# Kernel optimization log

Measured on AMD Instinct MI355X. Metric: run time of the kernel, lower is better.

The kernel has to match this reference:

```python
import jax, jax.numpy as jnp
import numpy as np

IMAGE_SIZE = 256
NEAR = 0.1
FAR = 100.0
EPS = 1e-3
BACKGROUND = (0.0, 0.0, 0.0)
CHUNK = 64   # faces per scan step (bounds peak memory of the z-buffer pass)
TINY = 1e-12


def _bary(vx, vy, vz, xp, yp):
    """Barycentric weights / perspective-correct depth at pixel centers.
    vx, vy, vz: 3-tuples of vertex coords, broadcastable with xp/yp.
    Mirrors the CUDA kernel: unnormalized cross-product weights, normalize,
    clamp to [0,1], renormalize, zp = 1 / sum(w_k / z_k), near/far clip."""
    x0, x1, x2 = vx; y0, y1, y2 = vy; z0, z1, z2 = vz
    w0 = yp * (x2 - x1) + xp * (y1 - y2) + (x1 * y2 - x2 * y1)
    w1 = yp * (x0 - x2) + xp * (y2 - y0) + (x2 * y0 - x0 * y2)
    w2 = yp * (x1 - x0) + xp * (y0 - y1) + (x0 * y1 - x1 * y0)
    det = w0 + w1 + w2
    safe_det = jnp.where(jnp.abs(det) > TINY, det, 1.0)
    n0, n1, n2 = w0 / safe_det, w1 / safe_det, w2 / safe_det
    inside = (n0 > 0) & (n1 > 0) & (n2 > 0) & (jnp.abs(det) > TINY)
    n0 = jnp.clip(n0, 0.0, 1.0); n1 = jnp.clip(n1, 0.0, 1.0); n2 = jnp.clip(n2, 0.0, 1.0)
    s = n0 + n1 + n2
    s = jnp.where(s > TINY, s, 1.0)
    n0, n1, n2 = n0 / s, n1 / s, n2 / s
    inv_zp = n0 / z0 + n1 / z1 + n2 / z2
    inv_zp = jnp.where(jnp.abs(inv_zp) > TINY, inv_zp, 1.0)
    zp = 1.0 / inv_zp
    valid = inside & (zp > NEAR) & (zp < FAR)
    return (n0, n1, n2), zp, valid


def _pixel_coords():
    IS = IMAGE_SIZE
    return (2.0 * jnp.arange(IS, dtype=jnp.float32) + 1.0 - IS) / IS


def _forward(faces, textures):
    B, F = faces.shape[:2]
    IS = IMAGE_SIZE
    ii = _pixel_coords()

    # ---- pass 1: z-buffer (face-index argmin), chunked scan over faces ----
    # index selection is non-differentiable -> stop_gradient keeps vjp cheap
    fsg = jax.lax.stop_gradient(faces)
    n_chunks = F // CHUNK
    fchunks = jnp.transpose(fsg.reshape(B, n_chunks, CHUNK, 3, 3), (1, 0, 2, 3, 4))
    bases = jnp.arange(n_chunks, dtype=jnp.int32) * CHUNK
    xp4 = ii[None, None, None, :]
    yp4 = ii[None, None, :, None]

    def step(carry, inp):
        depth, fidx = carry
        fc, base = inp                               # fc: [B, CHUNK, 3, 3]
        vx = tuple(fc[:, :, k, 0][:, :, None, None] for k in range(3))
        vy = tuple(fc[:, :, k, 1][:, :, None, None] for k in range(3))
        vz = tuple(fc[:, :, k, 2][:, :, None, None] for k in range(3))
        _, zp, valid = _bary(vx, vy, vz, xp4, yp4)   # [B, CHUNK, IS, IS]
        zp = jnp.where(valid, zp, jnp.inf)
        local = jnp.argmin(zp, axis=1).astype(jnp.int32)
        zbest = jnp.min(zp, axis=1)
        better = zbest < depth
        depth = jnp.where(better, zbest, depth)
        fidx = jnp.where(better, base + local, fidx)
        return (depth, fidx), None

    init = (jnp.full((B, IS, IS), FAR, jnp.float32),
            jnp.full((B, IS, IS), -1, jnp.int32))
    (_, fidx), _ = jax.lax.scan(step, init, (fchunks, bases))

    # ---- pass 2: differentiable recompute for winning faces ----
    mask = fidx >= 0
    safe_idx = jnp.maximum(fidx, 0)
    fsel = jnp.take_along_axis(
        faces.reshape(B, F, 9), safe_idx.reshape(B, -1, 1), axis=1
    ).reshape(B, IS, IS, 3, 3)
    vx = tuple(fsel[..., k, 0] for k in range(3))
    vy = tuple(fsel[..., k, 1] for k in range(3))
    vz = tuple(fsel[..., k, 2] for k in range(3))
    w, zp, _ = _bary(vx, vy, vz, ii[None, None, :], ii[None, :, None])
    depth_map = jnp.where(mask, zp, FAR)

    # ---- texture sampling: 8-corner trilinear in the T^3 face texel cube ----
    T = textures.shape[2]
    tif = [jnp.clip(w[k] * (T - 1) * zp / vz[k], 0.0, T - 1 - EPS) for k in range(3)]
    lo = [jnp.floor(t) for t in tif]
    fr = [t - l for t, l in zip(tif, lo)]
    lo = [l.astype(jnp.int32) for l in lo]

    tex_flat = textures.reshape(B, F * T * T * T, 3)
    base_idx = safe_idx * (T * T * T)
    rgb = jnp.zeros((B, IS, IS, 3), faces.dtype)
    for d0 in (0, 1):
        for d1 in (0, 1):
            for d2 in (0, 1):
                wgt = ((fr[0] if d0 else 1.0 - fr[0]) *
                       (fr[1] if d1 else 1.0 - fr[1]) *
                       (fr[2] if d2 else 1.0 - fr[2]))
                idx = base_idx + (lo[0] + d0) * T * T + (lo[1] + d1) * T + (lo[2] + d2)
                smp = jnp.take_along_axis(tex_flat, idx.reshape(B, -1, 1), axis=1)
                rgb = rgb + wgt[..., None] * smp.reshape(B, IS, IS, 3)

    bg = jnp.asarray(BACKGROUND, faces.dtype)
    mf = mask.astype(faces.dtype)[..., None]
    rgb_map = rgb * mf + (1.0 - mf) * bg
    alpha_map = mask.astype(faces.dtype)
    # pack (rgb, alpha, depth) into a single [B, IS, IS, 5] tensor
    return jnp.concatenate([rgb_map, alpha_map[..., None], depth_map[..., None]], axis=-1)


def setup_inputs() -> dict:
    key = jax.random.key(0)
    B, F, T = 4, 4096, 4
    k1, k2, k3, k4, k5 = jax.random.split(key, 5)
    # small triangles scattered over the screen with depths in (near, far)
    ctr = jax.random.uniform(k1, (B, F, 1, 2), minval=-0.95, maxval=0.95)
    off = jax.random.uniform(k2, (B, F, 3, 2), minval=-0.08, maxval=0.08)
    xy = ctr + off
    zc = jax.random.uniform(k3, (B, F, 1, 1), minval=1.0, maxval=50.0)
    zo = jax.random.uniform(k4, (B, F, 3, 1), minval=-0.2, maxval=0.2)
    faces = jnp.concatenate([xy, zc + zo], axis=-1).astype(jnp.float32)
    textures = jax.random.uniform(k5, (B, F, T, T, T, 3), dtype=jnp.float32)
    return {"faces": faces, "textures": textures}


def reference(faces, textures):
    return _forward(faces, textures)
```

## Files before the change

kernel.cpp:

```cpp
#include <hip/hip_runtime.h>

#define IS 256
#define FCOUNT 4096
#define NEARP 0.1f
#define FARP 100.0f
#define TINYF 1e-12f
#define CAP 192
#define GCAP 128
#define DET_GLOBAL 1e-5f
#define ZEPS 2e-4f

__device__ __forceinline__ float frn(float r) { asm("" : "+v"(r)); return r; }
__device__ __forceinline__ float mulrn(float a, float b) { return frn(a * b); }
__device__ __forceinline__ float addrn(float a, float b) { return frn(a + b); }
__device__ __forceinline__ float subrn(float a, float b) { return frn(a - b); }
__device__ __forceinline__ float divrn(float a, float b) { return frn(a / b); }
__device__ __forceinline__ float fmarn(float a, float b, float c) {
    return frn(__builtin_fmaf(a, b, c));
}

__global__ __launch_bounds__(64) void bin_kernel(
    const float* __restrict__ faces,
    float4* __restrict__ cA, float4* __restrict__ cB, float4* __restrict__ cC,
    int* __restrict__ counts, int* __restrict__ lists,
    int* __restrict__ gcount, int* __restrict__ glist, int B, int F)
{
    const int gid = blockIdx.x * 64 + threadIdx.x;
    if (gid >= B * F) return;
    const int b = gid >> 12, f = gid & (FCOUNT - 1);
    const float* fp = faces + (size_t)gid * 9;
    const float x0 = fp[0], y0 = fp[1], z0 = fp[2];
    const float x1 = fp[3], y1 = fp[4], z1 = fp[5];
    const float x2 = fp[6], y2 = fp[7], z2 = fp[8];

    const float A0 = subrn(x2, x1), B0 = subrn(y1, y2);
    const float C0 = fmarn(x1, y2, -mulrn(x2, y1));
    const float A1 = subrn(x0, x2), B1 = subrn(y2, y0);
    const float C1 = fmarn(x2, y0, -mulrn(x0, y2));
    const float A2 = subrn(x1, x0), B2 = subrn(y0, y1);
    const float C2 = fmarn(x0, y1, -mulrn(x1, y0));
    cA[gid] = make_float4(A0, B0, C0, A1);
    cB[gid] = make_float4(B1, C1, A2, B2);
    cC[gid] = make_float4(C2, z0, z1, z2);

    const float det = (x1 - x0) * (y2 - y0) - (x2 - x0) * (y1 - y0);
    const float ad = fabsf(det);
    if (ad < DET_GLOBAL) {
        const int pos = atomicAdd(&gcount[b], 1);
        if (pos < GCAP) glist[b * GCAP + pos] = f;
        return;
    }
    const float d = 2e-3f + 3e-7f / ad;
    const float lox = fminf(x0, fminf(x1, x2)) - d;
    const float hix = fmaxf(x0, fmaxf(x1, x2)) + d;
    const float loy = fminf(y0, fminf(y1, y2)) - d;
    const float hiy = fmaxf(y0, fmaxf(y1, y2)) + d;
    int tx0 = (int)ceilf ((256.f * lox + 241.f) * (1.f / 16.f));
    int tx1 = (int)floorf((256.f * hix + 255.f) * (1.f / 16.f));
    int ty0 = (int)ceilf ((256.f * loy + 241.f) * (1.f / 16.f));
    int ty1 = (int)floorf((256.f * hiy + 255.f) * (1.f / 16.f));
    tx0 = max(tx0, 0); tx1 = min(tx1, 31);
    ty0 = max(ty0, 0); ty1 = min(ty1, 31);
    for (int ty = ty0; ty <= ty1; ++ty)
        for (int tx = tx0; tx <= tx1; ++tx) {
            const int t = (b * 32 + ty) * 32 + tx;
            const int pos = atomicAdd(&counts[t], 1);
            if (pos < CAP) lists[(size_t)t * CAP + pos] = f;
        }
}

__global__ __launch_bounds__(256) void raster_kernel(
    const float* __restrict__ faces,
    const float* __restrict__ textures,
    const float4* __restrict__ cA, const float4* __restrict__ cB,
    const float4* __restrict__ cC,
    const int* __restrict__ counts, const int* __restrict__ lists,
    const int* __restrict__ gcount, const int* __restrict__ glist,
    float* __restrict__ out, int B, int F)
{
    const int tid  = threadIdx.x;
    const int lane = tid & 63;
    const int w    = tid >> 6;
    const int b    = blockIdx.x >> 8;
    const int tile = blockIdx.x & 255;
    const int qtx  = 2 * (tile & 15) + (w & 1);
    const int qty  = 2 * (tile >> 4) + (w >> 1);
    const int qbin = (b * 32 + qty) * 32 + qtx;
    const int px   = qtx * 8 + (lane & 7);
    const int py   = qty * 8 + (lane >> 3);
    const float xp = (float)(2 * px + 1 - IS) * (1.0f / IS);
    const float yp = (float)(2 * py + 1 - IS) * (1.0f / IS);

    __shared__ float4 s_a[4][64];
    __shared__ float4 s_b[4][64];
    __shared__ float4 s_c[4][64];
    __shared__ int    s_i[4][64];

    float bestz = FARP;
    int   besti = -1;

    const int cnt  = min(counts[qbin], CAP);
    const int gcnt = min(gcount[b], GCAP);
    const int total = cnt + gcnt;
    const int* mylist = lists + (size_t)qbin * CAP;
    const int* gl     = glist + b * GCAP;
    const int fb = b * F;

    for (int cb = 0; cb < total; cb += 64) {
        const int m = min(total - cb, 64);
        if (lane < m) {
            const int k = cb + lane;
            const int f = (k < cnt) ? mylist[k] : gl[k - cnt];
            s_a[w][lane] = cA[fb + f];
            s_b[w][lane] = cB[fb + f];
            s_c[w][lane] = cC[fb + f];
            s_i[w][lane] = f;
        }
        __builtin_amdgcn_wave_barrier();

        for (int j = 0; j < m; ++j) {
            const float4 fa  = s_a[w][j];
            const float4 fb4 = s_b[w][j];
            const float4 fc  = s_c[w][j];
            const float w0 = addrn(fmarn(yp, fa.x, mulrn(xp, fa.y)), fa.z);
            const float w1 = addrn(fmarn(yp, fa.w, mulrn(xp, fb4.x)), fb4.y);
            const float w2 = addrn(fmarn(yp, fb4.z, mulrn(xp, fb4.w)), fc.x);
            const float det = addrn(addrn(w0, w1), w2);
            bool ins;
            if (det > TINYF)       ins = (w0 > 0.f) && (w1 > 0.f) && (w2 > 0.f);
            else if (det < -TINYF) ins = (w0 < 0.f) && (w1 < 0.f) && (w2 < 0.f);
            else                   ins = false;
            const float minz = fminf(fminf(fc.y, fc.z), fc.w);
            if (ins && minz <= bestz + ZEPS) {
                float n0 = divrn(w0, det), n1 = divrn(w1, det), n2 = divrn(w2, det);
                n0 = frn(fminf(fmaxf(n0, 0.f), 1.f));
                n1 = frn(fminf(fmaxf(n1, 0.f), 1.f));
                n2 = frn(fminf(fmaxf(n2, 0.f), 1.f));
                float s = addrn(addrn(n0, n1), n2);
                s = (s > TINYF) ? s : 1.0f;
                n0 = divrn(n0, s); n1 = divrn(n1, s); n2 = divrn(n2, s);
                float iz = addrn(addrn(divrn(n0, fc.y), divrn(n1, fc.z)),
                                 divrn(n2, fc.w));
                iz = (fabsf(iz) > TINYF) ? iz : 1.0f;
                const float zp = divrn(1.0f, iz);
                if (zp > NEARP && zp < FARP) {
                    const int fi = s_i[w][j];
                    if (zp < bestz || (zp == bestz && fi < besti)) {
                        bestz = zp;
                        besti = fi;
                    }
                }
            }
        }
        __builtin_amdgcn_wave_barrier();
    }

    const float* fbase = faces + (size_t)b * F * 9;
    float r = 0.f, g = 0.f, bch = 0.f, alpha = 0.f, depth = FARP;
    if (besti >= 0) {
        const float* fp = fbase + (size_t)besti * 9;
        const float x0 = fp[0], y0 = fp[1], z0 = fp[2];
        const float x1 = fp[3], y1 = fp[4], z1 = fp[5];
        const float x2 = fp[6], y2 = fp[7], z2 = fp[8];
        const float w0 = addrn(fmarn(yp, subrn(x2, x1), mulrn(xp, subrn(y1, y2))),
                               fmarn(x1, y2, -mulrn(x2, y1)));
        const float w1 = addrn(fmarn(yp, subrn(x0, x2), mulrn(xp, subrn(y2, y0))),
                               fmarn(x2, y0, -mulrn(x0, y2)));
        const float w2 = addrn(fmarn(yp, subrn(x1, x0), mulrn(xp, subrn(y0, y1))),
                               fmarn(x0, y1, -mulrn(x1, y0)));
        const float det = addrn(addrn(w0, w1), w2);
        const float sd = (fabsf(det) > TINYF) ? det : 1.0f;
        float n0 = divrn(w0, sd), n1 = divrn(w1, sd), n2 = divrn(w2, sd);
        n0 = frn(fminf(fmaxf(n0, 0.f), 1.f));
        n1 = frn(fminf(fmaxf(n1, 0.f), 1.f));
        n2 = frn(fminf(fmaxf(n2, 0.f), 1.f));
        float s = addrn(addrn(n0, n1), n2);
        s = (s > TINYF) ? s : 1.0f;
        n0 = divrn(n0, s); n1 = divrn(n1, s); n2 = divrn(n2, s);
        float iz = addrn(addrn(divrn(n0, z0), divrn(n1, z1)), divrn(n2, z2));
        iz = (fabsf(iz) > TINYF) ? iz : 1.0f;
        const float zp = divrn(1.0f, iz);
        depth = zp;

        const float t0 = fminf(fmaxf(divrn(mulrn(mulrn(n0, 3.0f), zp), z0), 0.f), 2.999f);
        const float t1 = fminf(fmaxf(divrn(mulrn(mulrn(n1, 3.0f), zp), z1), 0.f), 2.999f);
        const float t2 = fminf(fmaxf(divrn(mulrn(mulrn(n2, 3.0f), zp), z2), 0.f), 2.999f);
        const float l0 = floorf(t0), l1 = floorf(t1), l2 = floorf(t2);
        const float fr0 = subrn(t0, l0), fr1 = subrn(t1, l1), fr2 = subrn(t2, l2);
        const int i0 = (int)l0, i1 = (int)l1, i2 = (int)l2;

        const float* tx = textures + (size_t)(b * F + besti) * 64 * 3;
        for (int d0 = 0; d0 < 2; ++d0)
            for (int d1 = 0; d1 < 2; ++d1)
                for (int d2 = 0; d2 < 2; ++d2) {
                    const float wg = mulrn(mulrn(d0 ? fr0 : subrn(1.0f, fr0),
                                                 d1 ? fr1 : subrn(1.0f, fr1)),
                                           d2 ? fr2 : subrn(1.0f, fr2));
                    const float* tp = tx + ((i0 + d0) * 16 + (i1 + d1) * 4 + (i2 + d2)) * 3;
                    r   = addrn(r,   mulrn(wg, tp[0]));
                    g   = addrn(g,   mulrn(wg, tp[1]));
                    bch = addrn(bch, mulrn(wg, tp[2]));
                }
        alpha = 1.0f;
    }

    float* op = out + (((size_t)b * IS + py) * IS + px) * 5;
    op[0] = r;
    op[1] = g;
    op[2] = bch;
    op[3] = alpha;
    op[4] = depth;
}

extern "C" void kernel_launch(void* const* d_in, const int* in_sizes, int n_in,
                              void* d_out, int out_size, void* d_ws, size_t ws_size,
                              hipStream_t stream) {
    const float* faces    = (const float*)d_in[0];
    const float* textures = (const float*)d_in[1];
    float* out = (float*)d_out;
    const int F = FCOUNT;
    const int B = in_sizes[0] / (F * 9);
    const int nbins = B * 1024;

    int* counts = (int*)d_ws;
    int* gcount = counts + nbins;
    int* glist  = gcount + B;
    int* lists  = glist + B * GCAP;
    float4* cA  = (float4*)(lists + (size_t)nbins * CAP);
    float4* cB  = cA + (size_t)B * F;
    float4* cC  = cB + (size_t)B * F;

    hipMemsetAsync(counts, 0, (size_t)(nbins + B) * sizeof(int), stream);
    bin_kernel<<<dim3((B * F + 63) / 64), dim3(64), 0, stream>>>(
        faces, cA, cB, cC, counts, lists, gcount, glist, B, F);
    raster_kernel<<<dim3(B * 256), dim3(256), 0, stream>>>(
        faces, textures, cA, cB, cC, counts, lists, gcount, glist, out, B, F);
}
```

Baseline: 99.83 us.

## Fuse memset, binning and raster into one cooperative kernel with grid syncs

Replaces the memset plus two kernel launches with a single cooperative kernel. It zeroes the bin counters, bins the faces with a grid-stride loop, then rasterizes, separating the phases with grid-wide barriers. The aim is to remove launch gaps and inter-kernel drain between the small stages. In exchange it adds two grid syncs and needs all 1024 blocks co-resident (launch_bounds 256,4), which can fail or limit occupancy.

```diff
diff --git a/kernel.cpp b/kernel.cpp
--- a/kernel.cpp
+++ b/kernel.cpp
@@ -1,4 +1,7 @@
 #include <hip/hip_runtime.h>
+#include <hip/hip_cooperative_groups.h>
+
+namespace cg = cooperative_groups;
 
 #define IS 256
 #define FCOUNT 4096
@@ -19,66 +22,68 @@
     return frn(__builtin_fmaf(a, b, c));
 }
 
-__global__ __launch_bounds__(64) void bin_kernel(
+__global__ __launch_bounds__(256, 4) void fused_kernel(
     const float* __restrict__ faces,
+    const float* __restrict__ textures,
     float4* __restrict__ cA, float4* __restrict__ cB, float4* __restrict__ cC,
     int* __restrict__ counts, int* __restrict__ lists,
-    int* __restrict__ gcount, int* __restrict__ glist, int B, int F)
-{
-    const int gid = blockIdx.x * 64 + threadIdx.x;
-    if (gid >= B * F) return;
-    const int b = gid >> 12, f = gid & (FCOUNT - 1);
-    const float* fp = faces + (size_t)gid * 9;
-    const float x0 = fp[0], y0 = fp[1], z0 = fp[2];
-    const float x1 = fp[3], y1 = fp[4], z1 = fp[5];
-    const float x2 = fp[6], y2 = fp[7], z2 = fp[8];
-
-    const float A0 = subrn(x2, x1), B0 = subrn(y1, y2);
-    const float C0 = fmarn(x1, y2, -mulrn(x2, y1));
-    const float A1 = subrn(x0, x2), B1 = subrn(y2, y0);
-    const float C1 = fmarn(x2, y0, -mulrn(x0, y2));
-    const float A2 = subrn(x1, x0), B2 = subrn(y0, y1);
-    const float C2 = fmarn(x0, y1, -mulrn(x1, y0));
-    cA[gid] = make_float4(A0, B0, C0, A1);
-    cB[gid] = make_float4(B1, C1, A2, B2);
-    cC[gid] = make_float4(C2, z0, z1, z2);
-
-    const float det = (x1 - x0) * (y2 - y0) - (x2 - x0) * (y1 - y0);
-    const float ad = fabsf(det);
-    if (ad < DET_GLOBAL) {
-        const int pos = atomicAdd(&gcount[b], 1);
-        if (pos < GCAP) glist[b * GCAP + pos] = f;
-        return;
-    }
-    const float d = 2e-3f + 3e-7f / ad;
-    const float lox = fminf(x0, fminf(x1, x2)) - d;
-    const float hix = fmaxf(x0, fmaxf(x1, x2)) + d;
-    const float loy = fminf(y0, fminf(y1, y2)) - d;
-    const float hiy = fmaxf(y0, fmaxf(y1, y2)) + d;
-    int tx0 = (int)ceilf ((256.f * lox + 241.f) * (1.f / 16.f));
-    int tx1 = (int)floorf((256.f * hix + 255.f) * (1.f / 16.f));
-    int ty0 = (int)ceilf ((256.f * loy + 241.f) * (1.f / 16.f));
-    int ty1 = (int)floorf((256.f * hiy + 255.f) * (1.f / 16.f));
-    tx0 = max(tx0, 0); tx1 = min(tx1, 31);
-    ty0 = max(ty0, 0); ty1 = min(ty1, 31);
-    for (int ty = ty0; ty <= ty1; ++ty)
-        for (int tx = tx0; tx <= tx1; ++tx) {
-            const int t = (b * 32 + ty) * 32 + tx;
-            const int pos = atomicAdd(&counts[t], 1);
-            if (pos < CAP) lists[(size_t)t * CAP + pos] = f;
-        }
-}
-
-__global__ __launch_bounds__(256) void raster_kernel(
-    const float* __restrict__ faces,
-    const float* __restrict__ textures,
-    const float4* __restrict__ cA, const float4* __restrict__ cB,
-    const float4* __restrict__ cC,
-    const int* __restrict__ counts, const int* __restrict__ lists,
-    const int* __restrict__ gcount, const int* __restrict__ glist,
+    int* __restrict__ gcount, int* __restrict__ glist,
     float* __restrict__ out, int B, int F)
 {
-    const int tid  = threadIdx.x;
+    const int tid      = threadIdx.x;
+    const int gid      = blockIdx.x * 256 + tid;
+    const int nthreads = gridDim.x * 256;
+    const int nbins    = B * 1024;
+
+    for (int i = gid; i < nbins + B; i += nthreads) counts[i] = 0;
+
+    cg::this_grid().sync();
+
+    for (int fg = gid; fg < B * F; fg += nthreads) {
+        const int b = fg >> 12, f = fg & (FCOUNT - 1);
+        const float* fp = faces + (size_t)fg * 9;
+        const float x0 = fp[0], y0 = fp[1], z0 = fp[2];
+        const float x1 = fp[3], y1 = fp[4], z1 = fp[5];
+        const float x2 = fp[6], y2 = fp[7], z2 = fp[8];
+
+        const float A0 = subrn(x2, x1), B0 = subrn(y1, y2);
+        const float C0 = fmarn(x1, y2, -mulrn(x2, y1));
+        const float A1 = subrn(x0, x2), B1 = subrn(y2, y0);
+        const float C1 = fmarn(x2, y0, -mulrn(x0, y2));
+        const float A2 = subrn(x1, x0), B2 = subrn(y0, y1);
+        const float C2 = fmarn(x0, y1, -mulrn(x1, y0));
+        cA[fg] = make_float4(A0, B0, C0, A1);
+        cB[fg] = make_float4(B1, C1, A2, B2);
+        cC[fg] = make_float4(C2, z0, z1, z2);
+
+        const float det = (x1 - x0) * (y2 - y0) - (x2 - x0) * (y1 - y0);
+        const float ad = fabsf(det);
+        if (ad < DET_GLOBAL) {
+            const int pos = atomicAdd(&gcount[b], 1);
+            if (pos < GCAP) glist[b * GCAP + pos] = f;
+        } else {
+            const float d = 2e-3f + 3e-7f / ad;
+            const float lox = fminf(x0, fminf(x1, x2)) - d;
+            const float hix = fmaxf(x0, fmaxf(x1, x2)) + d;
+            const float loy = fminf(y0, fminf(y1, y2)) - d;
+            const float hiy = fmaxf(y0, fmaxf(y1, y2)) + d;
+            int tx0 = (int)ceilf ((256.f * lox + 241.f) * (1.f / 16.f));
+            int tx1 = (int)floorf((256.f * hix + 255.f) * (1.f / 16.f));
+            int ty0 = (int)ceilf ((256.f * loy + 241.f) * (1.f / 16.f));
+            int ty1 = (int)floorf((256.f * hiy + 255.f) * (1.f / 16.f));
+            tx0 = max(tx0, 0); tx1 = min(tx1, 31);
+            ty0 = max(ty0, 0); ty1 = min(ty1, 31);
+            for (int ty = ty0; ty <= ty1; ++ty)
+                for (int tx = tx0; tx <= tx1; ++tx) {
+                    const int t = (b * 32 + ty) * 32 + tx;
+                    const int pos = atomicAdd(&counts[t], 1);
+                    if (pos < CAP) lists[(size_t)t * CAP + pos] = f;
+                }
+        }
+    }
+
+    cg::this_grid().sync();
+
     const int lane = tid & 63;
     const int w    = tid >> 6;
     const int b    = blockIdx.x >> 8;
@@ -230,9 +235,13 @@
     float4* cB  = cA + (size_t)B * F;
     float4* cC  = cB + (size_t)B * F;
 
-    hipMemsetAsync(counts, 0, (size_t)(nbins + B) * sizeof(int), stream);
-    bin_kernel<<<dim3((B * F + 63) / 64), dim3(64), 0, stream>>>(
-        faces, cA, cB, cC, counts, lists, gcount, glist, B, F);
-    raster_kernel<<<dim3(B * 256), dim3(256), 0, stream>>>(
-        faces, textures, cA, cB, cC, counts, lists, gcount, glist, out, B, F);
+    int Bv = B, Fv = F;
+    void* args[] = {
+        (void*)&faces, (void*)&textures,
+        (void*)&cA, (void*)&cB, (void*)&cC,
+        (void*)&counts, (void*)&lists, (void*)&gcount, (void*)&glist,
+        (void*)&out, (void*)&Bv, (void*)&Fv
+    };
+    hipLaunchCooperativeKernel((const void*)fused_kernel,
+                               dim3(B * 256), dim3(256), args, 0, stream);
 }
```

Result: slower. 255.8 us (+156.2%).

## Fuse binning into raster kernel with per-block shared-memory face culling

Applied to the files above, without the earlier changes.

Removes the separate memset and global binning kernel with its atomics. Each 256-thread block now scans all 4096 faces of its image, culls them against its 32x32 pixel tile, and stores passing faces in shared memory with a 4-bit quadrant mask. Each wave then loops over that shared list and skips faces whose mask bit does not cover its own 8x8 quadrant. This drops two launches and the global list traffic, but every block re-reads all faces (about 1024 blocks times 147KB) and the per-tile cap of 320 may silently drop faces.

```diff
diff --git a/kernel.cpp b/kernel.cpp
--- a/kernel.cpp
+++ b/kernel.cpp
@@ -5,8 +5,7 @@
 #define NEARP 0.1f
 #define FARP 100.0f
 #define TINYF 1e-12f
-#define CAP 192
-#define GCAP 128
+#define CAP_T 320
 #define DET_GLOBAL 1e-5f
 #define ZEPS 2e-4f
 
@@ -19,63 +18,9 @@
     return frn(__builtin_fmaf(a, b, c));
 }
 
-__global__ __launch_bounds__(64) void bin_kernel(
-    const float* __restrict__ faces,
-    float4* __restrict__ cA, float4* __restrict__ cB, float4* __restrict__ cC,
-    int* __restrict__ counts, int* __restrict__ lists,
-    int* __restrict__ gcount, int* __restrict__ glist, int B, int F)
-{
-    const int gid = blockIdx.x * 64 + threadIdx.x;
-    if (gid >= B * F) return;
-    const int b = gid >> 12, f = gid & (FCOUNT - 1);
-    const float* fp = faces + (size_t)gid * 9;
-    const float x0 = fp[0], y0 = fp[1], z0 = fp[2];
-    const float x1 = fp[3], y1 = fp[4], z1 = fp[5];
-    const float x2 = fp[6], y2 = fp[7], z2 = fp[8];
-
-    const float A0 = subrn(x2, x1), B0 = subrn(y1, y2);
-    const float C0 = fmarn(x1, y2, -mulrn(x2, y1));
-    const float A1 = subrn(x0, x2), B1 = subrn(y2, y0);
-    const float C1 = fmarn(x2, y0, -mulrn(x0, y2));
-    const float A2 = subrn(x1, x0), B2 = subrn(y0, y1);
-    const float C2 = fmarn(x0, y1, -mulrn(x1, y0));
-    cA[gid] = make_float4(A0, B0, C0, A1);
-    cB[gid] = make_float4(B1, C1, A2, B2);
-    cC[gid] = make_float4(C2, z0, z1, z2);
-
-    const float det = (x1 - x0) * (y2 - y0) - (x2 - x0) * (y1 - y0);
-    const float ad = fabsf(det);
-    if (ad < DET_GLOBAL) {
-        const int pos = atomicAdd(&gcount[b], 1);
-        if (pos < GCAP) glist[b * GCAP + pos] = f;
-        return;
-    }
-    const float d = 2e-3f + 3e-7f / ad;
-    const float lox = fminf(x0, fminf(x1, x2)) - d;
-    const float hix = fmaxf(x0, fmaxf(x1, x2)) + d;
-    const float loy = fminf(y0, fminf(y1, y2)) - d;
-    const float hiy = fmaxf(y0, fmaxf(y1, y2)) + d;
-    int tx0 = (int)ceilf ((256.f * lox + 241.f) * (1.f / 16.f));
-    int tx1 = (int)floorf((256.f * hix + 255.f) * (1.f / 16.f));
-    int ty0 = (int)ceilf ((256.f * loy + 241.f) * (1.f / 16.f));
-    int ty1 = (int)floorf((256.f * hiy + 255.f) * (1.f / 16.f));
-    tx0 = max(tx0, 0); tx1 = min(tx1, 31);
-    ty0 = max(ty0, 0); ty1 = min(ty1, 31);
-    for (int ty = ty0; ty <= ty1; ++ty)
-        for (int tx = tx0; tx <= tx1; ++tx) {
-            const int t = (b * 32 + ty) * 32 + tx;
-            const int pos = atomicAdd(&counts[t], 1);
-            if (pos < CAP) lists[(size_t)t * CAP + pos] = f;
-        }
-}
-
-__global__ __launch_bounds__(256) void raster_kernel(
+__global__ __launch_bounds__(256, 4) void fused_raster(
     const float* __restrict__ faces,
     const float* __restrict__ textures,
-    const float4* __restrict__ cA, const float4* __restrict__ cB,
-    const float4* __restrict__ cC,
-    const int* __restrict__ counts, const int* __restrict__ lists,
-    const int* __restrict__ gcount, const int* __restrict__ glist,
     float* __restrict__ out, int B, int F)
 {
     const int tid  = threadIdx.x;
@@ -83,82 +28,122 @@
     const int w    = tid >> 6;
     const int b    = blockIdx.x >> 8;
     const int tile = blockIdx.x & 255;
-    const int qtx  = 2 * (tile & 15) + (w & 1);
-    const int qty  = 2 * (tile >> 4) + (w >> 1);
-    const int qbin = (b * 32 + qty) * 32 + qtx;
-    const int px   = qtx * 8 + (lane & 7);
-    const int py   = qty * 8 + (lane >> 3);
+    const int TX   = tile & 15;
+    const int TY   = tile >> 4;
+
+    __shared__ float4 s_a[CAP_T];
+    __shared__ float4 s_b[CAP_T];
+    __shared__ float4 s_c[CAP_T];
+    __shared__ int    s_i[CAP_T];
+    __shared__ int    s_cnt;
+
+    if (tid == 0) s_cnt = 0;
+    __syncthreads();
+
+    const float qxlo0 = (float)(32 * TX +  1 - 256) * (1.0f / 256.0f);
+    const float qxhi0 = (float)(32 * TX + 15 - 256) * (1.0f / 256.0f);
+    const float qxlo1 = (float)(32 * TX + 17 - 256) * (1.0f / 256.0f);
+    const float qxhi1 = (float)(32 * TX + 31 - 256) * (1.0f / 256.0f);
+    const float qylo0 = (float)(32 * TY +  1 - 256) * (1.0f / 256.0f);
+    const float qyhi0 = (float)(32 * TY + 15 - 256) * (1.0f / 256.0f);
+    const float qylo1 = (float)(32 * TY + 17 - 256) * (1.0f / 256.0f);
+    const float qyhi1 = (float)(32 * TY + 31 - 256) * (1.0f / 256.0f);
+
+    const float* fimg = faces + (size_t)b * F * 9;
+    for (int f = tid; f < F; f += 256) {
+        const float* fp = fimg + (size_t)f * 9;
+        const float x0 = fp[0], y0 = fp[1], z0 = fp[2];
+        const float x1 = fp[3], y1 = fp[4], z1 = fp[5];
+        const float x2 = fp[6], y2 = fp[7], z2 = fp[8];
+
+        const float det = (x1 - x0) * (y2 - y0) - (x2 - x0) * (y1 - y0);
+        const float ad = fabsf(det);
+        int mask;
+        if (ad < DET_GLOBAL) {
+            mask = 0xF;
+        } else {
+            const float d = 2e-3f + 3e-7f / ad;
+            const float lox = fminf(x0, fminf(x1, x2)) - d;
+            const float hix = fmaxf(x0, fmaxf(x1, x2)) + d;
+            const float loy = fminf(y0, fminf(y1, y2)) - d;
+            const float hiy = fmaxf(y0, fmaxf(y1, y2)) + d;
+            const bool ox0 = (hix >= qxlo0) && (lox <= qxhi0);
+            const bool ox1 = (hix >= qxlo1) && (lox <= qxhi1);
+            const bool oy0 = (hiy >= qylo0) && (loy <= qyhi0);
+            const bool oy1 = (hiy >= qylo1) && (loy <= qyhi1);
+            mask = ((ox0 && oy0) ? 1 : 0) | ((ox1 && oy0) ? 2 : 0)
+                 | ((ox0 && oy1) ? 4 : 0) | ((ox1 && oy1) ? 8 : 0);
+        }
+        if (mask) {
+            const float A0 = subrn(x2, x1), B0 = subrn(y1, y2);
+            const float C0 = fmarn(x1, y2, -mulrn(x2, y1));
+            const float A1 = subrn(x0, x2), B1 = subrn(y2, y0);
+            const float C1 = fmarn(x2, y0, -mulrn(x0, y2));
+            const float A2 = subrn(x1, x0), B2 = subrn(y0, y1);
+            const float C2 = fmarn(x0, y1, -mulrn(x1, y0));
+            const int pos = atomicAdd(&s_cnt, 1);
+            if (pos < CAP_T) {
+                s_a[pos] = make_float4(A0, B0, C0, A1);
+                s_b[pos] = make_float4(B1, C1, A2, B2);
+                s_c[pos] = make_float4(C2, z0, z1, z2);
+                s_i[pos] = f | (mask << 12);
+            }
+        }
+    }
+    __syncthreads();
+    const int cnt = min(s_cnt, CAP_T);
+
+    const int qtx = 2 * TX + (w & 1);
+    const int qty = 2 * TY + (w >> 1);
+    const int px  = qtx * 8 + (lane & 7);
+    const int py  = qty * 8 + (lane >> 3);
     const float xp = (float)(2 * px + 1 - IS) * (1.0f / IS);
     const float yp = (float)(2 * py + 1 - IS) * (1.0f / IS);
-
-    __shared__ float4 s_a[4][64];
-    __shared__ float4 s_b[4][64];
-    __shared__ float4 s_c[4][64];
-    __shared__ int    s_i[4][64];
+    const int qbit = 1 << (12 + w);
 
     float bestz = FARP;
     int   besti = -1;
 
-    const int cnt  = min(counts[qbin], CAP);
-    const int gcnt = min(gcount[b], GCAP);
-    const int total = cnt + gcnt;
-    const int* mylist = lists + (size_t)qbin * CAP;
-    const int* gl     = glist + b * GCAP;
-    const int fb = b * F;
-
-    for (int cb = 0; cb < total; cb += 64) {
-        const int m = min(total - cb, 64);
-        if (lane < m) {
-            const int k = cb + lane;
-            const int f = (k < cnt) ? mylist[k] : gl[k - cnt];
-            s_a[w][lane] = cA[fb + f];
-            s_b[w][lane] = cB[fb + f];
-            s_c[w][lane] = cC[fb + f];
-            s_i[w][lane] = f;
-        }
-        __builtin_amdgcn_wave_barrier();
-
-        for (int j = 0; j < m; ++j) {
-            const float4 fa  = s_a[w][j];
-            const float4 fb4 = s_b[w][j];
-            const float4 fc  = s_c[w][j];
-            const float w0 = addrn(fmarn(yp, fa.x, mulrn(xp, fa.y)), fa.z);
-            const float w1 = addrn(fmarn(yp, fa.w, mulrn(xp, fb4.x)), fb4.y);
-            const float w2 = addrn(fmarn(yp, fb4.z, mulrn(xp, fb4.w)), fc.x);
-            const float det = addrn(addrn(w0, w1), w2);
-            bool ins;
-            if (det > TINYF)       ins = (w0 > 0.f) && (w1 > 0.f) && (w2 > 0.f);
-            else if (det < -TINYF) ins = (w0 < 0.f) && (w1 < 0.f) && (w2 < 0.f);
-            else                   ins = false;
-            const float minz = fminf(fminf(fc.y, fc.z), fc.w);
-            if (ins && minz <= bestz + ZEPS) {
-                float n0 = divrn(w0, det), n1 = divrn(w1, det), n2 = divrn(w2, det);
-                n0 = frn(fminf(fmaxf(n0, 0.f), 1.f));
-                n1 = frn(fminf(fmaxf(n1, 0.f), 1.f));
-                n2 = frn(fminf(fmaxf(n2, 0.f), 1.f));
-                float s = addrn(addrn(n0, n1), n2);
-                s = (s > TINYF) ? s : 1.0f;
-                n0 = divrn(n0, s); n1 = divrn(n1, s); n2 = divrn(n2, s);
-                float iz = addrn(addrn(divrn(n0, fc.y), divrn(n1, fc.z)),
-                                 divrn(n2, fc.w));
-                iz = (fabsf(iz) > TINYF) ? iz : 1.0f;
-                const float zp = divrn(1.0f, iz);
-                if (zp > NEARP && zp < FARP) {
-                    const int fi = s_i[w][j];
-                    if (zp < bestz || (zp == bestz && fi < besti)) {
-                        bestz = zp;
-                        besti = fi;
-                    }
+    for (int j = 0; j < cnt; ++j) {
+        const int mi = s_i[j];
+        if (!(mi & qbit)) continue;
+        const float4 fa  = s_a[j];
+        const float4 fb4 = s_b[j];
+        const float4 fc  = s_c[j];
+        const float w0 = addrn(fmarn(yp, fa.x, mulrn(xp, fa.y)), fa.z);
+        const float w1 = addrn(fmarn(yp, fa.w, mulrn(xp, fb4.x)), fb4.y);
+        const float w2 = addrn(fmarn(yp, fb4.z, mulrn(xp, fb4.w)), fc.x);
+        const float det = addrn(addrn(w0, w1), w2);
+        bool ins;
+        if (det > TINYF)       ins = (w0 > 0.f) && (w1 > 0.f) && (w2 > 0.f);
+        else if (det < -TINYF) ins = (w0 < 0.f) && (w1 < 0.f) && (w2 < 0.f);
+        else                   ins = false;
+        const float minz = fminf(fminf(fc.y, fc.z), fc.w);
+        if (ins && minz <= bestz + ZEPS) {
+            float n0 = divrn(w0, det), n1 = divrn(w1, det), n2 = divrn(w2, det);
+            n0 = frn(fminf(fmaxf(n0, 0.f), 1.f));
+            n1 = frn(fminf(fmaxf(n1, 0.f), 1.f));
+            n2 = frn(fminf(fmaxf(n2, 0.f), 1.f));
+            float s = addrn(addrn(n0, n1), n2);
+            s = (s > TINYF) ? s : 1.0f;
+            n0 = divrn(n0, s); n1 = divrn(n1, s); n2 = divrn(n2, s);
+            float iz = addrn(addrn(divrn(n0, fc.y), divrn(n1, fc.z)),
+                             divrn(n2, fc.w));
+            iz = (fabsf(iz) > TINYF) ? iz : 1.0f;
+            const float zp = divrn(1.0f, iz);
+            if (zp > NEARP && zp < FARP) {
+                const int fi = mi & 0xFFF;
+                if (zp < bestz || (zp == bestz && fi < besti)) {
+                    bestz = zp;
+                    besti = fi;
                 }
             }
         }
-        __builtin_amdgcn_wave_barrier();
     }
 
-    const float* fbase = faces + (size_t)b * F * 9;
     float r = 0.f, g = 0.f, bch = 0.f, alpha = 0.f, depth = FARP;
     if (besti >= 0) {
-        const float* fp = fbase + (size_t)besti * 9;
+        const float* fp = fimg + (size_t)besti * 9;
         const float x0 = fp[0], y0 = fp[1], z0 = fp[2];
         const float x1 = fp[3], y1 = fp[4], z1 = fp[5];
         const float x2 = fp[6], y2 = fp[7], z2 = fp[8];
@@ -220,19 +205,7 @@
     float* out = (float*)d_out;
     const int F = FCOUNT;
     const int B = in_sizes[0] / (F * 9);
-    const int nbins = B * 1024;
-
-    int* counts = (int*)d_ws;
-    int* gcount = counts + nbins;
-    int* glist  = gcount + B;
-    int* lists  = glist + B * GCAP;
-    float4* cA  = (float4*)(lists + (size_t)nbins * CAP);
-    float4* cB  = cA + (size_t)B * F;
-    float4* cC  = cB + (size_t)B * F;
-
-    hipMemsetAsync(counts, 0, (size_t)(nbins + B) * sizeof(int), stream);
-    bin_kernel<<<dim3((B * F + 63) / 64), dim3(64), 0, stream>>>(
-        faces, cA, cB, cC, counts, lists, gcount, glist, B, F);
-    raster_kernel<<<dim3(B * 256), dim3(256), 0, stream>>>(
-        faces, textures, cA, cB, cC, counts, lists, gcount, glist, out, B, F);
+
+    fused_raster<<<dim3(B * 256), dim3(256), 0, stream>>>(
+        faces, textures, out, B, F);
 }
```

Result: faster. 96.64 us (median of 2 runs) (-3.2%).

## Stage face loads via LDS in binning, prefetch per-face coefficients in raster

Applied to the files above, without the earlier changes.

The bin kernel now loads each 64-face block's vertex data into shared memory with coalesced float4 loads instead of strided 9-float per-thread reads. The raster kernel switches to one 64-thread block per 8x8 bin and drops the LDS staging and wave barriers. Each face's coefficients are read through uniform global loads with a one-face-ahead software prefetch. The winning face's barycentrics and depths are kept in registers, so the second barycentric recompute from the raw faces is removed. The risks are that the per-face global loads sit on the critical loop with only one face of lookahead, and that each thread now holds more registers.

```diff
diff --git a/kernel.cpp b/kernel.cpp
--- a/kernel.cpp
+++ b/kernel.cpp
@@ -19,16 +19,29 @@
     return frn(__builtin_fmaf(a, b, c));
 }
 
+
 __global__ __launch_bounds__(64) void bin_kernel(
     const float* __restrict__ faces,
     float4* __restrict__ cA, float4* __restrict__ cB, float4* __restrict__ cC,
     int* __restrict__ counts, int* __restrict__ lists,
     int* __restrict__ gcount, int* __restrict__ glist, int B, int F)
 {
-    const int gid = blockIdx.x * 64 + threadIdx.x;
+    const int lane = threadIdx.x;
+    const int base = blockIdx.x * 64;
+    const int gid  = base + lane;
     if (gid >= B * F) return;
     const int b = gid >> 12, f = gid & (FCOUNT - 1);
-    const float* fp = faces + (size_t)gid * 9;
+
+    __shared__ float4 stage4[144];
+    float* stage = (float*)stage4;
+    const float* src = faces + (size_t)base * 9;
+    const float4* s4 = (const float4*)src;
+    stage4[lane]      = s4[lane];
+    stage4[64 + lane] = s4[64 + lane];
+    stage[512 + lane] = src[512 + lane];
+    __builtin_amdgcn_wave_barrier();
+
+    const float* fp = stage + lane * 9;
     const float x0 = fp[0], y0 = fp[1], z0 = fp[2];
     const float x1 = fp[3], y1 = fp[4], z1 = fp[5];
     const float x2 = fp[6], y2 = fp[7], z2 = fp[8];
@@ -69,8 +82,7 @@
         }
 }
 
-__global__ __launch_bounds__(256) void raster_kernel(
-    const float* __restrict__ faces,
+__global__ __launch_bounds__(64) void raster_kernel(
     const float* __restrict__ textures,
     const float4* __restrict__ cA, const float4* __restrict__ cB,
     const float4* __restrict__ cC,
@@ -78,125 +90,96 @@
     const int* __restrict__ gcount, const int* __restrict__ glist,
     float* __restrict__ out, int B, int F)
 {
-    const int tid  = threadIdx.x;
-    const int lane = tid & 63;
-    const int w    = tid >> 6;
-    const int b    = blockIdx.x >> 8;
-    const int tile = blockIdx.x & 255;
-    const int qtx  = 2 * (tile & 15) + (w & 1);
-    const int qty  = 2 * (tile >> 4) + (w >> 1);
-    const int qbin = (b * 32 + qty) * 32 + qtx;
-    const int px   = qtx * 8 + (lane & 7);
-    const int py   = qty * 8 + (lane >> 3);
+    const int lane = threadIdx.x;
+    const int blk  = blockIdx.x;
+    const int b    = blk >> 10;
+    const int tx   = blk & 31;
+    const int ty   = (blk >> 5) & 31;
+    const int bin  = (b * 32 + ty) * 32 + tx;
+    const int px   = tx * 8 + (lane & 7);
+    const int py   = ty * 8 + (lane >> 3);
     const float xp = (float)(2 * px + 1 - IS) * (1.0f / IS);
     const float yp = (float)(2 * py + 1 - IS) * (1.0f / IS);
 
-    __shared__ float4 s_a[4][64];
-    __shared__ float4 s_b[4][64];
-    __shared__ float4 s_c[4][64];
-    __shared__ int    s_i[4][64];
+    const int cnt   = min(counts[bin], CAP);
+    const int gcnt  = min(gcount[b], GCAP);
+    const int total = cnt + gcnt;
+    const int* mylist = lists + (size_t)bin * CAP;
+    const int* gl     = glist + b * GCAP;
+    const int fb = b * F;
 
     float bestz = FARP;
     int   besti = -1;
-
-    const int cnt  = min(counts[qbin], CAP);
-    const int gcnt = min(gcount[b], GCAP);
-    const int total = cnt + gcnt;
-    const int* mylist = lists + (size_t)qbin * CAP;
-    const int* gl     = glist + b * GCAP;
-    const int fb = b * F;
-
-    for (int cb = 0; cb < total; cb += 64) {
-        const int m = min(total - cb, 64);
-        if (lane < m) {
-            const int k = cb + lane;
-            const int f = (k < cnt) ? mylist[k] : gl[k - cnt];
-            s_a[w][lane] = cA[fb + f];
-            s_b[w][lane] = cB[fb + f];
-            s_c[w][lane] = cC[fb + f];
-            s_i[w][lane] = f;
+    float bn0 = 0.f, bn1 = 0.f, bn2 = 0.f;
+    float bz0 = 1.f, bz1 = 1.f, bz2 = 1.f;
+
+    int    pf = 0;
+    float4 pa, pb, pc;
+    if (total > 0) {
+        pf = (0 < cnt) ? mylist[0] : gl[0];
+        pa = cA[fb + pf]; pb = cB[fb + pf]; pc = cC[fb + pf];
+    }
+    for (int j = 0; j < total; ++j) {
+        const float4 fa  = pa;
+        const float4 fb4 = pb;
+        const float4 fc  = pc;
+        const int    fi  = pf;
+        const int jn = j + 1;
+        if (jn < total) {
+            pf = (jn < cnt) ? mylist[jn] : gl[jn - cnt];
+            pa = cA[fb + pf]; pb = cB[fb + pf]; pc = cC[fb + pf];
         }
-        __builtin_amdgcn_wave_barrier();
-
-        for (int j = 0; j < m; ++j) {
-            const float4 fa  = s_a[w][j];
-            const float4 fb4 = s_b[w][j];
-            const float4 fc  = s_c[w][j];
-            const float w0 = addrn(fmarn(yp, fa.x, mulrn(xp, fa.y)), fa.z);
-            const float w1 = addrn(fmarn(yp, fa.w, mulrn(xp, fb4.x)), fb4.y);
-            const float w2 = addrn(fmarn(yp, fb4.z, mulrn(xp, fb4.w)), fc.x);
-            const float det = addrn(addrn(w0, w1), w2);
-            bool ins;
-            if (det > TINYF)       ins = (w0 > 0.f) && (w1 > 0.f) && (w2 > 0.f);
-            else if (det < -TINYF) ins = (w0 < 0.f) && (w1 < 0.f) && (w2 < 0.f);
-            else                   ins = false;
-            const float minz = fminf(fminf(fc.y, fc.z), fc.w);
-            if (ins && minz <= bestz + ZEPS) {
-                float n0 = divrn(w0, det), n1 = divrn(w1, det), n2 = divrn(w2, det);
-                n0 = frn(fminf(fmaxf(n0, 0.f), 1.f));
-                n1 = frn(fminf(fmaxf(n1, 0.f), 1.f));
-                n2 = frn(fminf(fmaxf(n2, 0.f), 1.f));
-                float s = addrn(addrn(n0, n1), n2);
-                s = (s > TINYF) ? s : 1.0f;
-                n0 = divrn(n0, s); n1 = divrn(n1, s); n2 = divrn(n2, s);
-                float iz = addrn(addrn(divrn(n0, fc.y), divrn(n1, fc.z)),
-                                 divrn(n2, fc.w));
-                iz = (fabsf(iz) > TINYF) ? iz : 1.0f;
-                const float zp = divrn(1.0f, iz);
-                if (zp > NEARP && zp < FARP) {
-                    const int fi = s_i[w][j];
-                    if (zp < bestz || (zp == bestz && fi < besti)) {
-                        bestz = zp;
-                        besti = fi;
-                    }
+        const float w0 = addrn(fmarn(yp, fa.x, mulrn(xp, fa.y)), fa.z);
+        const float w1 = addrn(fmarn(yp, fa.w, mulrn(xp, fb4.x)), fb4.y);
+        const float w2 = addrn(fmarn(yp, fb4.z, mulrn(xp, fb4.w)), fc.x);
+        const float det = addrn(addrn(w0, w1), w2);
+        bool ins;
+        if (det > TINYF)       ins = (w0 > 0.f) && (w1 > 0.f) && (w2 > 0.f);
+        else if (det < -TINYF) ins = (w0 < 0.f) && (w1 < 0.f) && (w2 < 0.f);
+        else                   ins = false;
+        const float minz = fminf(fminf(fc.y, fc.z), fc.w);
+        if (ins && minz <= bestz + ZEPS) {
+            float n0 = divrn(w0, det), n1 = divrn(w1, det), n2 = divrn(w2, det);
+            n0 = frn(fminf(fmaxf(n0, 0.f), 1.f));
+            n1 = frn(fminf(fmaxf(n1, 0.f), 1.f));
+            n2 = frn(fminf(fmaxf(n2, 0.f), 1.f));
+            float s = addrn(addrn(n0, n1), n2);
+            s = (s > TINYF) ? s : 1.0f;
+            n0 = divrn(n0, s); n1 = divrn(n1, s); n2 = divrn(n2, s);
+            float iz = addrn(addrn(divrn(n0, fc.y), divrn(n1, fc.z)),
+                             divrn(n2, fc.w));
+            iz = (fabsf(iz) > TINYF) ? iz : 1.0f;
+            const float zp = divrn(1.0f, iz);
+            if (zp > NEARP && zp < FARP) {
+                if (zp < bestz || (zp == bestz && fi < besti)) {
+                    bestz = zp;
+                    besti = fi;
+                    bn0 = n0; bn1 = n1; bn2 = n2;
+                    bz0 = fc.y; bz1 = fc.z; bz2 = fc.w;
                 }
             }
         }
-        __builtin_amdgcn_wave_barrier();
-    }
-
-    const float* fbase = faces + (size_t)b * F * 9;
+    }
+
     float r = 0.f, g = 0.f, bch = 0.f, alpha = 0.f, depth = FARP;
     if (besti >= 0) {
-        const float* fp = fbase + (size_t)besti * 9;
-        const float x0 = fp[0], y0 = fp[1], z0 = fp[2];
-        const float x1 = fp[3], y1 = fp[4], z1 = fp[5];
-        const float x2 = fp[6], y2 = fp[7], z2 = fp[8];
-        const float w0 = addrn(fmarn(yp, subrn(x2, x1), mulrn(xp, subrn(y1, y2))),
-                               fmarn(x1, y2, -mulrn(x2, y1)));
-        const float w1 = addrn(fmarn(yp, subrn(x0, x2), mulrn(xp, subrn(y2, y0))),
-                               fmarn(x2, y0, -mulrn(x0, y2)));
-        const float w2 = addrn(fmarn(yp, subrn(x1, x0), mulrn(xp, subrn(y0, y1))),
-                               fmarn(x0, y1, -mulrn(x1, y0)));
-        const float det = addrn(addrn(w0, w1), w2);
-        const float sd = (fabsf(det) > TINYF) ? det : 1.0f;
-        float n0 = divrn(w0, sd), n1 = divrn(w1, sd), n2 = divrn(w2, sd);
-        n0 = frn(fminf(fmaxf(n0, 0.f), 1.f));
-        n1 = frn(fminf(fmaxf(n1, 0.f), 1.f));
-        n2 = frn(fminf(fmaxf(n2, 0.f), 1.f));
-        float s = addrn(addrn(n0, n1), n2);
-        s = (s > TINYF) ? s : 1.0f;
-        n0 = divrn(n0, s); n1 = divrn(n1, s); n2 = divrn(n2, s);
-        float iz = addrn(addrn(divrn(n0, z0), divrn(n1, z1)), divrn(n2, z2));
-        iz = (fabsf(iz) > TINYF) ? iz : 1.0f;
-        const float zp = divrn(1.0f, iz);
+        const float zp = bestz;
         depth = zp;
-
-        const float t0 = fminf(fmaxf(divrn(mulrn(mulrn(n0, 3.0f), zp), z0), 0.f), 2.999f);
-        const float t1 = fminf(fmaxf(divrn(mulrn(mulrn(n1, 3.0f), zp), z1), 0.f), 2.999f);
-        const float t2 = fminf(fmaxf(divrn(mulrn(mulrn(n2, 3.0f), zp), z2), 0.f), 2.999f);
+        const float t0 = fminf(fmaxf(divrn(mulrn(mulrn(bn0, 3.0f), zp), bz0), 0.f), 2.999f);
+        const float t1 = fminf(fmaxf(divrn(mulrn(mulrn(bn1, 3.0f), zp), bz1), 0.f), 2.999f);
+        const float t2 = fminf(fmaxf(divrn(mulrn(mulrn(bn2, 3.0f), zp), bz2), 0.f), 2.999f);
         const float l0 = floorf(t0), l1 = floorf(t1), l2 = floorf(t2);
         const float fr0 = subrn(t0, l0), fr1 = subrn(t1, l1), fr2 = subrn(t2, l2);
         const int i0 = (int)l0, i1 = (int)l1, i2 = (int)l2;
 
-        const float* tx = textures + (size_t)(b * F + besti) * 64 * 3;
+        const float* txp = textures + (size_t)(b * F + besti) * 64 * 3;
         for (int d0 = 0; d0 < 2; ++d0)
             for (int d1 = 0; d1 < 2; ++d1)
                 for (int d2 = 0; d2 < 2; ++d2) {
                     const float wg = mulrn(mulrn(d0 ? fr0 : subrn(1.0f, fr0),
                                                  d1 ? fr1 : subrn(1.0f, fr1)),
                                            d2 ? fr2 : subrn(1.0f, fr2));
-                    const float* tp = tx + ((i0 + d0) * 16 + (i1 + d1) * 4 + (i2 + d2)) * 3;
+                    const float* tp = txp + ((i0 + d0) * 16 + (i1 + d1) * 4 + (i2 + d2)) * 3;
                     r   = addrn(r,   mulrn(wg, tp[0]));
                     g   = addrn(g,   mulrn(wg, tp[1]));
                     bch = addrn(bch, mulrn(wg, tp[2]));
@@ -233,6 +216,6 @@
     hipMemsetAsync(counts, 0, (size_t)(nbins + B) * sizeof(int), stream);
     bin_kernel<<<dim3((B * F + 63) / 64), dim3(64), 0, stream>>>(
         faces, cA, cB, cC, counts, lists, gcount, glist, B, F);
-    raster_kernel<<<dim3(B * 256), dim3(256), 0, stream>>>(
-        faces, textures, cA, cB, cC, counts, lists, gcount, glist, out, B, F);
-}
+    raster_kernel<<<dim3(B * 1024), dim3(64), 0, stream>>>(
+        textures, cA, cB, cC, counts, lists, gcount, glist, out, B, F);
+}
```

New measurement: 103.7 us. +3.9%, slower.
